# Kernel tuning notes

Measured on AMD Instinct MI355X. Metric: run time of the kernel, lower is better.

The kernel has to match this reference:

```python
import jax, jax.numpy as jnp
import numpy as np

D_MODEL = 512
NUM_HEADS = 8
HEAD_DIM = D_MODEL // NUM_HEADS
MAX_REL = 2


def setup_inputs() -> dict:
    key = jax.random.key(0)
    ks = jax.random.split(key, 12)
    B, S = 2, 4096
    std = 1.0 / np.sqrt(D_MODEL)
    inp = {
        'q': jax.random.normal(ks[0], (B, S, D_MODEL), jnp.float32),
        'k': jax.random.normal(ks[1], (B, S, D_MODEL), jnp.float32),
        'v': jax.random.normal(ks[2], (B, S, D_MODEL), jnp.float32),
        'Wq': jax.random.normal(ks[3], (D_MODEL, D_MODEL), jnp.float32) * std,
        'bq': jnp.zeros((D_MODEL,), jnp.float32),
        'Wk': jax.random.normal(ks[4], (D_MODEL, D_MODEL), jnp.float32) * std,
        'bk': jnp.zeros((D_MODEL,), jnp.float32),
        'Wv': jax.random.normal(ks[5], (D_MODEL, D_MODEL), jnp.float32) * std,
        'bv': jnp.zeros((D_MODEL,), jnp.float32),
        'Wo': jax.random.normal(ks[6], (D_MODEL, D_MODEL), jnp.float32) * std,
        'bo': jnp.zeros((D_MODEL,), jnp.float32),
        'rel_pos': jax.random.normal(ks[7], (NUM_HEADS, 2 * MAX_REL + 1), jnp.float32),
    }
    return inp


def _rel_bias(rel_pos, seq_len):
    pos = jnp.arange(seq_len)
    rel = pos[None, :] - pos[:, None]              # [S,S]
    idx = jnp.clip(rel, -MAX_REL, MAX_REL) + MAX_REL
    return rel_pos[:, idx]                         # [H,S,S]


def reference(q, k, v, Wq, bq, Wk, bk, Wv, bv, Wo, bo, rel_pos):
    B, S, D = q.shape
    H, Hd = NUM_HEADS, HEAD_DIM
    # torch Linear: x @ W.T + b
    Q = (q @ Wq.T + bq).reshape(B, S, H, Hd).transpose(0, 2, 1, 3)  # [B,H,S,Hd]
    K = (k @ Wk.T + bk).reshape(B, S, H, Hd).transpose(0, 2, 1, 3)
    V = (v @ Wv.T + bv).reshape(B, S, H, Hd).transpose(0, 2, 1, 3)
    scores = jnp.einsum('bhqd,bhkd->bhqk', Q, K) / jnp.sqrt(jnp.float32(Hd))
    scores = scores + _rel_bias(rel_pos, S)[None]                  # [B,H,S,S]
    probs = jax.nn.softmax(scores, axis=-1)
    attn = jnp.einsum('bhqk,bhkd->bhqd', probs, V)                 # [B,H,S,Hd]
    attn = attn.transpose(0, 2, 1, 3).reshape(B, S, D)
    return attn @ Wo.T + bo
```

## Files before the change

### kernel.cpp

```cpp
#include <hip/hip_runtime.h>

typedef __bf16 bf16_t;
typedef __bf16 bf16x2 __attribute__((ext_vector_type(2)));
typedef __bf16 bf16x4 __attribute__((ext_vector_type(4)));
typedef __bf16 bf16x8 __attribute__((ext_vector_type(8)));
typedef float f32x4 __attribute__((ext_vector_type(4)));
typedef unsigned int u32x4 __attribute__((ext_vector_type(4)));

#define MFMA16(a, b, c) __builtin_amdgcn_mfma_f32_16x16x32_bf16(a, b, c, 0, 0, 0)
#define LOG2E 1.4426950408889634f
#define SHIFT 16.0f

#define GLL(g, l)                                                      \
  __builtin_amdgcn_global_load_lds(                                    \
      (const __attribute__((address_space(1))) void*)(g),              \
      (__attribute__((address_space(3))) void*)(l), 16, 0, 0)

#define WAIT_BARRIER_V0() asm volatile("s_waitcnt vmcnt(0)\n\ts_barrier" ::: "memory")
#define WAIT_BARRIER_V6() asm volatile("s_waitcnt vmcnt(6)\n\ts_barrier" ::: "memory")

static constexpr int NB = 2;
static constexpr int SEQ = 4096;
static constexpr int DM = 512;
static constexpr int NH = 8;
static constexpr int HD = 64;
static constexpr int M_ROWS = NB * SEQ;

__global__ __launch_bounds__(256) void cvt_w_kernel(
    const float* __restrict__ w0, const float* __restrict__ w1,
    const float* __restrict__ w2, const float* __restrict__ w3,
    bf16_t* __restrict__ out) {
  const float* src = (blockIdx.y == 0) ? w0 : (blockIdx.y == 1) ? w1
                   : (blockIdx.y == 2) ? w2 : w3;
  int i = (blockIdx.x * 256 + threadIdx.x) * 4;
  float4 v = *(const float4*)(src + i);
  bf16_t* o = out + blockIdx.y * (DM * DM) + i;
  o[0] = (bf16_t)v.x; o[1] = (bf16_t)v.y; o[2] = (bf16_t)v.z; o[3] = (bf16_t)v.w;
}

__global__ __launch_bounds__(256) void cvt_x_kernel(
    const float* __restrict__ q, const float* __restrict__ k,
    const float* __restrict__ v, bf16_t* __restrict__ out) {
  const float* src = (blockIdx.y == 0) ? q : (blockIdx.y == 1) ? k : v;
  bf16_t* dst = out + (size_t)blockIdx.y * (M_ROWS * DM);
  int i = (blockIdx.x * 256 + threadIdx.x) * 8;
  float4 a = *(const float4*)(src + i);
  float4 b = *(const float4*)(src + i + 4);
  bf16x8 o;
  o[0] = (bf16_t)a.x; o[1] = (bf16_t)a.y; o[2] = (bf16_t)a.z; o[3] = (bf16_t)a.w;
  o[4] = (bf16_t)b.x; o[5] = (bf16_t)b.y; o[6] = (bf16_t)b.z; o[7] = (bf16_t)b.w;
  *(bf16x8*)(dst + i) = o;
}

__device__ __forceinline__ void gemm_body64(
    const bf16_t* __restrict__ X, const bf16_t* __restrict__ Wm,
    const float* __restrict__ bias, void* __restrict__ Out,
    int omode, float scale) {
  __shared__ bf16_t Asm[3][64 * 64];
  __shared__ bf16_t Bsm[3][128 * 64];

  const int tid = threadIdx.x;
  const int w = tid >> 6;
  const int lane = tid & 63;
  const int quad = lane >> 4, l15 = lane & 15;
  const int l8 = lane >> 3;
  const int swcol = ((lane & 7) ^ l8) * 8;
  const int m0 = blockIdx.x * 64;
  const int n0 = blockIdx.y * 128;
  const int moff = (w & 1) * 32;
  const int noff = (w >> 1) * 64;

  f32x4 acc[2][4];
#pragma unroll
  for (int mb = 0; mb < 2; mb++)
#pragma unroll
    for (int nb = 0; nb < 4; nb++) { acc[mb][nb][0] = 0.f; acc[mb][nb][1] = 0.f; acc[mb][nb][2] = 0.f; acc[mb][nb][3] = 0.f; }

  auto stage = [&](int ks, int bufi) {
    const int k0 = ks * 64;
#pragma unroll
    for (int j = 0; j < 4; j++) {
      const int row = j * 32 + w * 8 + l8;
      GLL(Wm + (size_t)(n0 + row) * DM + k0 + swcol, &Bsm[bufi][(j * 256 + w * 64) * 8]);
    }
#pragma unroll
    for (int j = 0; j < 2; j++) {
      const int row = j * 32 + w * 8 + l8;
      GLL(X + (size_t)(m0 + row) * DM + k0 + swcol, &Asm[bufi][(j * 256 + w * 64) * 8]);
    }
  };

  stage(0, 0);
  stage(1, 1);

  for (int ks = 0; ks < 8; ks++) {
    WAIT_BARRIER_V6();
    const int tn = (ks + 2 < 8) ? ks + 2 : 7;
    stage(tn, (ks + 2) % 3);
    const int p = ks % 3;

#pragma unroll
    for (int kd = 0; kd < 2; kd++) {
      const int fch = (((kd << 2) + quad) ^ (l15 & 7)) << 3;
      bf16x8 bfr[4];
#pragma unroll
      for (int nb = 0; nb < 4; nb++)
        bfr[nb] = *(const bf16x8*)&Bsm[p][(noff + nb * 16 + l15) * 64 + fch];
#pragma unroll
      for (int mb = 0; mb < 2; mb++) {
        bf16x8 a = *(const bf16x8*)&Asm[p][(moff + mb * 16 + l15) * 64 + fch];
#pragma unroll
        for (int nb = 0; nb < 4; nb++) acc[mb][nb] = MFMA16(a, bfr[nb], acc[mb][nb]);
      }
    }
  }

#pragma unroll
  for (int nb = 0; nb < 4; nb++) {
    const int n = n0 + noff + nb * 16 + l15;
    const float bn = bias[n];
    const int h = n >> 6, dd = n & 63;
#pragma unroll
    for (int mb = 0; mb < 2; mb++) {
      const int mbase = m0 + moff + mb * 16 + quad * 4;
      const int bb = mbase >> 12, s = mbase & 4095;
      if (omode == 0) {
#pragma unroll
        for (int r = 0; r < 4; r++) {
          const float val = (acc[mb][nb][r] + bn) * scale;
          ((bf16_t*)Out)[(size_t)((bb * NH + h) * SEQ + s + r) * HD + dd] = (bf16_t)val;
        }
      } else if (omode == 1) {
        bf16x4 pk;
#pragma unroll
        for (int r = 0; r < 4; r++) pk[r] = (bf16_t)(acc[mb][nb][r] + bn);
        *(bf16x4*)&((bf16_t*)Out)[(((size_t)(bb * NH + h) * HD + dd) << 12) + s] = pk;
      } else {
#pragma unroll
        for (int r = 0; r < 4; r++)
          ((float*)Out)[(size_t)(mbase + r) * DM + n] = acc[mb][nb][r] + bn;
      }
    }
  }
}

__global__ __launch_bounds__(256, 2) void qkv_kernel(
    const bf16_t* __restrict__ Xall, const bf16_t* __restrict__ Wall,
    const float* __restrict__ bq, const float* __restrict__ bk,
    const float* __restrict__ bv, bf16_t* __restrict__ Qb,
    bf16_t* __restrict__ Kb, bf16_t* __restrict__ Vb, float qscale) {
  const int z = blockIdx.z;
  const bf16_t* X = Xall + (size_t)z * (M_ROWS * DM);
  const float* bias = (z == 0) ? bq : (z == 1) ? bk : bv;
  bf16_t* Out = (z == 0) ? Qb : (z == 1) ? Kb : Vb;
  gemm_body64(X, Wall + (size_t)z * DM * DM, bias, Out,
              (z == 2) ? 1 : 0, (z == 0) ? qscale : 1.0f);
}

__global__ __launch_bounds__(256, 2) void oproj_kernel(
    const bf16_t* __restrict__ X, const bf16_t* __restrict__ Wm,
    const float* __restrict__ bias, float* __restrict__ Out) {
  gemm_body64(X, Wm, bias, Out, 2, 1.0f);
}

__global__ __launch_bounds__(256, 4) void attn_kernel(
    const bf16_t* __restrict__ Qb, const bf16_t* __restrict__ Kb,
    const bf16_t* __restrict__ Vb, const float* __restrict__ rel_pos,
    bf16_t* __restrict__ attn_out) {
  __shared__ bf16_t Kt[2][64 * 64];
  __shared__ bf16_t Vt[2][64 * 64];

  const int tid = threadIdx.x;
  const int w = tid >> 6;
  const int lane = tid & 63;
  const int quad = lane >> 4, l15 = lane & 15;
  const int wq = w >> 1, wk = w & 1;

  const int lin = blockIdx.x;
  const int glob = (lin & 7) * 128 + (lin >> 3);
  const int bh = glob >> 6;
  const int qb = glob & 63;
  const int b = bh >> 3, h = bh & 7;
  const int qlo = qb * 64 + wq * 32;

  const float rb0 = rel_pos[h * 5 + 0] * LOG2E;
  const float rb1 = rel_pos[h * 5 + 1] * LOG2E;
  const float rb2 = rel_pos[h * 5 + 2] * LOG2E;
  const float rb3 = rel_pos[h * 5 + 3] * LOG2E;
  const float rb4 = rel_pos[h * 5 + 4] * LOG2E;

  bf16x8 qf[2][2];
#pragma unroll
  for (int mb = 0; mb < 2; mb++)
#pragma unroll
    for (int kd = 0; kd < 2; kd++)
      qf[mb][kd] = *(const bf16x8*)(Qb + (size_t)(bh * SEQ + qlo + mb * 16 + l15) * HD + kd * 32 + 8 * quad);

  f32x4 o[2][4];
#pragma unroll
  for (int mb = 0; mb < 2; mb++)
#pragma unroll
    for (int db = 0; db < 4; db++) { o[mb][db][0] = 0.f; o[mb][db][1] = 0.f; o[mb][db][2] = 0.f; o[mb][db][3] = 0.f; }
  f32x4 l4[2];
  l4[0][0] = 0.f; l4[0][1] = 0.f; l4[0][2] = 0.f; l4[0][3] = 0.f;
  l4[1][0] = 0.f; l4[1][1] = 0.f; l4[1][2] = 0.f; l4[1][3] = 0.f;

  bf16x8 ones;
#pragma unroll
  for (int i = 0; i < 8; i++) ones[i] = (bf16_t)1.0f;

  const int srow = (w << 4) + (lane >> 3);
  const int scol = (((lane & 7) ^ (lane >> 3)) << 3);
  const bf16_t* kg0 = Kb + ((size_t)(bh * SEQ + srow) << 6) + scol;
  const bf16_t* vg0 = Vb + (((size_t)(bh * HD + srow)) << 12) + scol;
  const int ldst = (w << 10);

  const int sw = l15 & 7;
  const int kfo0 = (l15 << 6) + ((quad ^ sw) << 3);
  const int kfo1 = (l15 << 6) + (((quad + 4) ^ sw) << 3);
  const int vfo = (l15 << 6) + ((((wk << 2) + quad) ^ sw) << 3);
  const int wk2 = wk << 1;

  auto stage = [&](int t, int bufi) {
    GLL(kg0 + ((size_t)t << 12), &Kt[bufi][ldst]);
    GLL(kg0 + ((size_t)t << 12) + (8 << 6), &Kt[bufi][ldst + 512]);
    GLL(vg0 + (t << 6), &Vt[bufi][ldst]);
    GLL(vg0 + (t << 6) + (8 << 12), &Vt[bufi][ldst + 512]);
  };

  stage(0, 0);

  for (int t = 0; t < 64; t++) {
    WAIT_BARRIER_V0();
    if (t + 1 < 64) stage(t + 1, (t + 1) & 1);
    const int p = t & 1;
    const int klo = t * 64 + wk * 32;

    float cini;
    bool nearband = false;
    if (klo >= qlo + 33)        cini = rb4 - SHIFT;
    else if (klo <= qlo - 33)   cini = rb0 - SHIFT;
    else                        { cini = -SHIFT; nearband = true; }

    f32x4 s[2][2];
#pragma unroll
    for (int mb = 0; mb < 2; mb++)
#pragma unroll
      for (int kb = 0; kb < 2; kb++) { s[mb][kb][0] = cini; s[mb][kb][1] = cini; s[mb][kb][2] = cini; s[mb][kb][3] = cini; }
    __builtin_amdgcn_s_setprio(1);
#pragma unroll
    for (int kb = 0; kb < 2; kb++) {
      bf16x8 kA0 = *(const bf16x8*)&Kt[p][kfo0 + ((wk2 + kb) << 10)];
      bf16x8 kA1 = *(const bf16x8*)&Kt[p][kfo1 + ((wk2 + kb) << 10)];
      s[0][kb] = MFMA16(kA0, qf[0][0], s[0][kb]);
      s[0][kb] = MFMA16(kA1, qf[0][1], s[0][kb]);
      s[1][kb] = MFMA16(kA0, qf[1][0], s[1][kb]);
      s[1][kb] = MFMA16(kA1, qf[1][1], s[1][kb]);
    }
    __builtin_amdgcn_s_setprio(0);

    if (nearband) {
#pragma unroll
      for (int mb = 0; mb < 2; mb++) {
        const int qg = qlo + mb * 16 + l15;
#pragma unroll
        for (int kb = 0; kb < 2; kb++)
#pragma unroll
          for (int r = 0; r < 4; r++) {
            int dl = klo + kb * 16 + quad * 4 + r - qg;
            float bias = dl <= -2 ? rb0
                       : (dl >= 2 ? rb4
                       : (dl == -1 ? rb1 : (dl == 0 ? rb2 : rb3)));
            s[mb][kb][r] += bias;
          }
      }
    }

    bf16x8 pf[2];
#pragma unroll
    for (int mb = 0; mb < 2; mb++) {
      unsigned int u[2][2];
#pragma unroll
      for (int kb = 0; kb < 2; kb++) {
        bf16x2 p0, p1;
        p0[0] = (bf16_t)__builtin_amdgcn_exp2f(s[mb][kb][0]);
        p0[1] = (bf16_t)__builtin_amdgcn_exp2f(s[mb][kb][1]);
        p1[0] = (bf16_t)__builtin_amdgcn_exp2f(s[mb][kb][2]);
        p1[1] = (bf16_t)__builtin_amdgcn_exp2f(s[mb][kb][3]);
        u[kb][0] = __builtin_bit_cast(unsigned int, p0);
        u[kb][1] = __builtin_bit_cast(unsigned int, p1);
      }
      unsigned int a0 = u[0][0], b0 = u[1][0];
      unsigned int a1 = u[0][1], b1 = u[1][1];
      asm("v_permlane32_swap_b32 %0, %1" : "+v"(a0), "+v"(b0));
      asm("v_permlane32_swap_b32 %0, %1" : "+v"(a1), "+v"(b1));
      asm("v_permlane16_swap_b32 %0, %1" : "+v"(a0), "+v"(b0));
      asm("v_permlane16_swap_b32 %0, %1" : "+v"(a1), "+v"(b1));
      u32x4 pk; pk[0] = a0; pk[1] = a1; pk[2] = b0; pk[3] = b1;
      pf[mb] = __builtin_bit_cast(bf16x8, pk);
    }

    __builtin_amdgcn_s_setprio(1);
    l4[0] = MFMA16(ones, pf[0], l4[0]);
    l4[1] = MFMA16(ones, pf[1], l4[1]);
#pragma unroll
    for (int db = 0; db < 4; db++) {
      bf16x8 vA = *(const bf16x8*)&Vt[p][vfo + (db << 10)];
      o[0][db] = MFMA16(vA, pf[0], o[0][db]);
      o[1][db] = MFMA16(vA, pf[1], o[1][db]);
    }
    __builtin_amdgcn_s_setprio(0);
  }

  asm volatile("s_waitcnt vmcnt(0)" ::: "memory");
  __syncthreads();
  float* Ored = (float*)&Kt[0][0];
  float* lred = (float*)&Vt[0][0];
  if (wk) {
#pragma unroll
    for (int mb = 0; mb < 2; mb++) {
      lred[(wq << 5) + (mb << 4) + l15] = l4[mb][0];
#pragma unroll
      for (int db = 0; db < 4; db++) {
        const int ch = ((db << 2) | quad) ^ sw;
        *(f32x4*)&Ored[(wq << 11) + ((mb * 16 + l15) << 6) + (ch << 2)] = o[mb][db];
      }
    }
  }
  __syncthreads();
  if (!wk) {
#pragma unroll
    for (int mb = 0; mb < 2; mb++) {
      float lsum = l4[mb][0] + lred[(wq << 5) + (mb << 4) + l15];
      const float inv = 1.0f / lsum;
      const int qg = qlo + mb * 16 + l15;
#pragma unroll
      for (int db = 0; db < 4; db++) {
        const int ch = ((db << 2) | quad) ^ sw;
        const f32x4 part = *(const f32x4*)&Ored[(wq << 11) + ((mb * 16 + l15) << 6) + (ch << 2)];
        bf16x4 pk;
#pragma unroll
        for (int r = 0; r < 4; r++) pk[r] = (bf16_t)((o[mb][db][r] + part[r]) * inv);
        *(bf16x4*)(attn_out + (size_t)(b * SEQ + qg) * DM + h * HD + db * 16 + quad * 4) = pk;
      }
    }
  }
}

extern "C" void kernel_launch(void* const* d_in, const int* in_sizes, int n_in,
                              void* d_out, int out_size, void* d_ws, size_t ws_size,
                              hipStream_t stream) {
  const float* q   = (const float*)d_in[0];
  const float* k   = (const float*)d_in[1];
  const float* v   = (const float*)d_in[2];
  const float* Wq  = (const float*)d_in[3];
  const float* bq  = (const float*)d_in[4];
  const float* Wk  = (const float*)d_in[5];
  const float* bk  = (const float*)d_in[6];
  const float* Wv  = (const float*)d_in[7];
  const float* bv  = (const float*)d_in[8];
  const float* Wo  = (const float*)d_in[9];
  const float* bo  = (const float*)d_in[10];
  const float* rel = (const float*)d_in[11];

  char* ws = (char*)d_ws;
  bf16_t* Wbf  = (bf16_t*)ws;
  bf16_t* Xb   = (bf16_t*)(ws + (size_t)(2  << 20));
  bf16_t* Qbuf = (bf16_t*)(ws + (size_t)(26 << 20));
  bf16_t* Kbuf = (bf16_t*)(ws + (size_t)(34 << 20));
  bf16_t* Vbuf = (bf16_t*)(ws + (size_t)(42 << 20));
  bf16_t* Abuf = (bf16_t*)(ws + (size_t)(2  << 20));

  cvt_w_kernel<<<dim3(256, 4), 256, 0, stream>>>(Wq, Wk, Wv, Wo, Wbf);
  cvt_x_kernel<<<dim3(2048, 3), 256, 0, stream>>>(q, k, v, Xb);

  const float qscale = LOG2E / 8.0f;
  qkv_kernel<<<dim3(128, 4, 3), 256, 0, stream>>>(
      Xb, Wbf, bq, bk, bv, Qbuf, Kbuf, Vbuf, qscale);

  attn_kernel<<<1024, 256, 0, stream>>>(Qbuf, Kbuf, Vbuf, rel, Abuf);

  oproj_kernel<<<dim3(128, 4), 256, 0, stream>>>(Abuf, Wbf + 3 * DM * DM, bo, (float*)d_out);
}
```

Baseline: 233.9 us.

## Enlarge GEMM tiles to 128x128, double-buffer, and split attention launch

The shared projection GEMM body moves from a 64x128 tile with triple buffering to a 128x128 tile with double buffering, a full vmcnt(0) wait per k-step, and 4x4 MFMA accumulators per wave. This raises data reuse per loaded tile and halves the grid. The cost is less prefetch depth and fewer blocks (256 per z for qkv, 256 for oproj), which lowers occupancy and latency hiding. Attention is also split into two 512-block launches via a glob_base offset, which changes how blocks map to batch-head pairs and adds one launch.

Measured after the change: 259.4 us. +10.9%, slower.

```diff
diff --git a/kernel.cpp b/kernel.cpp
--- a/kernel.cpp
+++ b/kernel.cpp
@@ -17,7 +17,6 @@
       (__attribute__((address_space(3))) void*)(l), 16, 0, 0)
 
 #define WAIT_BARRIER_V0() asm volatile("s_waitcnt vmcnt(0)\n\ts_barrier" ::: "memory")
-#define WAIT_BARRIER_V6() asm volatile("s_waitcnt vmcnt(6)\n\ts_barrier" ::: "memory")
 
 static constexpr int NB = 2;
 static constexpr int SEQ = 4096;
@@ -52,12 +51,12 @@
   *(bf16x8*)(dst + i) = o;
 }
 
-__device__ __forceinline__ void gemm_body64(
+__device__ __forceinline__ void gemm_body128(
     const bf16_t* __restrict__ X, const bf16_t* __restrict__ Wm,
     const float* __restrict__ bias, void* __restrict__ Out,
     int omode, float scale) {
-  __shared__ bf16_t Asm[3][64 * 64];
-  __shared__ bf16_t Bsm[3][128 * 64];
+  __shared__ bf16_t Asm[2][128 * 64];
+  __shared__ bf16_t Bsm[2][128 * 64];
 
   const int tid = threadIdx.x;
   const int w = tid >> 6;
@@ -65,14 +64,14 @@
   const int quad = lane >> 4, l15 = lane & 15;
   const int l8 = lane >> 3;
   const int swcol = ((lane & 7) ^ l8) * 8;
-  const int m0 = blockIdx.x * 64;
+  const int m0 = blockIdx.x * 128;
   const int n0 = blockIdx.y * 128;
-  const int moff = (w & 1) * 32;
+  const int moff = (w & 1) * 64;
   const int noff = (w >> 1) * 64;
 
-  f32x4 acc[2][4];
-#pragma unroll
-  for (int mb = 0; mb < 2; mb++)
+  f32x4 acc[4][4];
+#pragma unroll
+  for (int mb = 0; mb < 4; mb++)
 #pragma unroll
     for (int nb = 0; nb < 4; nb++) { acc[mb][nb][0] = 0.f; acc[mb][nb][1] = 0.f; acc[mb][nb][2] = 0.f; acc[mb][nb][3] = 0.f; }
 
@@ -82,36 +81,32 @@
     for (int j = 0; j < 4; j++) {
       const int row = j * 32 + w * 8 + l8;
       GLL(Wm + (size_t)(n0 + row) * DM + k0 + swcol, &Bsm[bufi][(j * 256 + w * 64) * 8]);
-    }
-#pragma unroll
-    for (int j = 0; j < 2; j++) {
-      const int row = j * 32 + w * 8 + l8;
       GLL(X + (size_t)(m0 + row) * DM + k0 + swcol, &Asm[bufi][(j * 256 + w * 64) * 8]);
     }
   };
 
   stage(0, 0);
-  stage(1, 1);
 
   for (int ks = 0; ks < 8; ks++) {
-    WAIT_BARRIER_V6();
-    const int tn = (ks + 2 < 8) ? ks + 2 : 7;
-    stage(tn, (ks + 2) % 3);
-    const int p = ks % 3;
+    WAIT_BARRIER_V0();
+    if (ks + 1 < 8) stage(ks + 1, (ks + 1) & 1);
+    const int p = ks & 1;
 
 #pragma unroll
     for (int kd = 0; kd < 2; kd++) {
       const int fch = (((kd << 2) + quad) ^ (l15 & 7)) << 3;
-      bf16x8 bfr[4];
+      bf16x8 bfr[4], afr[4];
 #pragma unroll
       for (int nb = 0; nb < 4; nb++)
         bfr[nb] = *(const bf16x8*)&Bsm[p][(noff + nb * 16 + l15) * 64 + fch];
 #pragma unroll
-      for (int mb = 0; mb < 2; mb++) {
-        bf16x8 a = *(const bf16x8*)&Asm[p][(moff + mb * 16 + l15) * 64 + fch];
-#pragma unroll
-        for (int nb = 0; nb < 4; nb++) acc[mb][nb] = MFMA16(a, bfr[nb], acc[mb][nb]);
-      }
+      for (int mb = 0; mb < 4; mb++)
+        afr[mb] = *(const bf16x8*)&Asm[p][(moff + mb * 16 + l15) * 64 + fch];
+#pragma unroll
+      for (int mb = 0; mb < 4; mb++)
+#pragma unroll
+        for (int nb = 0; nb < 4; nb++)
+          acc[mb][nb] = MFMA16(afr[mb], bfr[nb], acc[mb][nb]);
     }
   }
 
@@ -121,7 +116,7 @@
     const float bn = bias[n];
     const int h = n >> 6, dd = n & 63;
 #pragma unroll
-    for (int mb = 0; mb < 2; mb++) {
+    for (int mb = 0; mb < 4; mb++) {
       const int mbase = m0 + moff + mb * 16 + quad * 4;
       const int bb = mbase >> 12, s = mbase & 4095;
       if (omode == 0) {
@@ -153,20 +148,20 @@
   const bf16_t* X = Xall + (size_t)z * (M_ROWS * DM);
   const float* bias = (z == 0) ? bq : (z == 1) ? bk : bv;
   bf16_t* Out = (z == 0) ? Qb : (z == 1) ? Kb : Vb;
-  gemm_body64(X, Wall + (size_t)z * DM * DM, bias, Out,
-              (z == 2) ? 1 : 0, (z == 0) ? qscale : 1.0f);
+  gemm_body128(X, Wall + (size_t)z * DM * DM, bias, Out,
+               (z == 2) ? 1 : 0, (z == 0) ? qscale : 1.0f);
 }
 
 __global__ __launch_bounds__(256, 2) void oproj_kernel(
     const bf16_t* __restrict__ X, const bf16_t* __restrict__ Wm,
     const float* __restrict__ bias, float* __restrict__ Out) {
-  gemm_body64(X, Wm, bias, Out, 2, 1.0f);
+  gemm_body128(X, Wm, bias, Out, 2, 1.0f);
 }
 
 __global__ __launch_bounds__(256, 4) void attn_kernel(
     const bf16_t* __restrict__ Qb, const bf16_t* __restrict__ Kb,
     const bf16_t* __restrict__ Vb, const float* __restrict__ rel_pos,
-    bf16_t* __restrict__ attn_out) {
+    bf16_t* __restrict__ attn_out, int glob_base) {
   __shared__ bf16_t Kt[2][64 * 64];
   __shared__ bf16_t Vt[2][64 * 64];
 
@@ -177,7 +172,7 @@
   const int wq = w >> 1, wk = w & 1;
 
   const int lin = blockIdx.x;
-  const int glob = (lin & 7) * 128 + (lin >> 3);
+  const int glob = glob_base + (lin & 7) * 64 + (lin >> 3);
   const int bh = glob >> 6;
   const int qb = glob & 63;
   const int b = bh >> 3, h = bh & 7;
@@ -375,10 +370,11 @@
   cvt_x_kernel<<<dim3(2048, 3), 256, 0, stream>>>(q, k, v, Xb);
 
   const float qscale = LOG2E / 8.0f;
-  qkv_kernel<<<dim3(128, 4, 3), 256, 0, stream>>>(
+  qkv_kernel<<<dim3(64, 4, 3), 256, 0, stream>>>(
       Xb, Wbf, bq, bk, bv, Qbuf, Kbuf, Vbuf, qscale);
 
-  attn_kernel<<<1024, 256, 0, stream>>>(Qbuf, Kbuf, Vbuf, rel, Abuf);
-
-  oproj_kernel<<<dim3(128, 4), 256, 0, stream>>>(Abuf, Wbf + 3 * DM * DM, bo, (float*)d_out);
-}
+  attn_kernel<<<512, 256, 0, stream>>>(Qbuf, Kbuf, Vbuf, rel, Abuf, 0);
+  attn_kernel<<<512, 256, 0, stream>>>(Qbuf, Kbuf, Vbuf, rel, Abuf, 512);
+
+  oproj_kernel<<<dim3(64, 4), 256, 0, stream>>>(Abuf, Wbf + 3 * DM * DM, bo, (float*)d_out);
+}
```
